# Kernel optimization log

Hardware: AMD Instinct MI355X
Metric: run time of the kernel (lower is better)

The kernel has to match this reference:

```python
import jax, jax.numpy as jnp
import numpy as np

N_NODES = 100000   # ntoken
D = 128            # ninp
N_EDGES = 1600000  # n_nodes * avg_degree(16)


def setup_inputs() -> dict:
    key = jax.random.key(0)
    k0, k1, k2, k3 = jax.random.split(key, 4)
    # nn.Embedding weight, xavier_normal_ init; row 0 is padding_idx -> zeros
    emb = jax.random.normal(k0, (N_NODES, D), jnp.float32) * np.float32(np.sqrt(2.0 / (N_NODES + D)))
    emb = emb.at[0].set(0.0)
    # GCNConv weights (glorot) and biases (zeros), as in torch_geometric defaults
    W1 = jax.random.normal(k1, (D, 2 * D), jnp.float32) * np.float32(np.sqrt(2.0 / (D + 2 * D)))
    b1 = jnp.zeros((2 * D,), jnp.float32)
    W2 = jax.random.normal(k2, (2 * D, D), jnp.float32) * np.float32(np.sqrt(2.0 / (2 * D + D)))
    b2 = jnp.zeros((D,), jnp.float32)
    edge_index = jax.random.randint(k3, (2, N_EDGES), 0, N_NODES, dtype=jnp.int64)
    return {"emb": emb, "W1": W1, "b1": b1, "W2": W2, "b2": b2, "edge_index": edge_index}


def gcn_conv(x, W, b, src, dst, n):
    """torch_geometric GCNConv: add self-loops, sym deg^{-1/2} norm, edge_weight=1."""
    h = x @ W  # [n, out]
    loop = jnp.arange(n, dtype=src.dtype)
    src2 = jnp.concatenate([src, loop])
    dst2 = jnp.concatenate([dst, loop])
    # degree computed at destination (col) including self-loops
    deg = jax.ops.segment_sum(jnp.ones_like(src2, dtype=h.dtype), dst2, num_segments=n)
    dinv = jnp.where(deg > 0, jax.lax.rsqrt(deg), 0.0)
    norm = dinv[src2] * dinv[dst2]  # [E+n]
    msg = h[src2] * norm[:, None]   # gather + scale (memory-bound)
    out = jax.ops.segment_sum(msg, dst2, num_segments=n)  # scatter-add
    return out + b


def reference(emb, W1, b1, W2, b2, edge_index):
    src, dst = edge_index[0], edge_index[1]
    n = emb.shape[0]
    h = gcn_conv(emb, W1, b1, src, dst, n)   # [N, 2D]; dropout = identity (eval)
    out = gcn_conv(h, W2, b2, src, dst, n)   # [N, D]
    return out
```

## Files before the change

### kernel.cpp

```cpp
#include <hip/hip_runtime.h>

static constexpr int D = 128;
static constexpr int CAP = 64;
static constexpr int NSLICE = 8;
static constexpr int CHUNK = 4096;

typedef __attribute__((ext_vector_type(8))) short bf16x8;
typedef __attribute__((ext_vector_type(4))) float f32x4;
typedef __attribute__((ext_vector_type(4))) int iv4;

__device__ inline unsigned bf16rne(float f) {
  unsigned u = __float_as_uint(f);
  return (u + 0x7FFFu + ((u >> 16) & 1u)) >> 16;
}

__global__ __launch_bounds__(256) void k_wprep(const float* __restrict__ W1,
                                               const float* __restrict__ W2,
                                               const float* __restrict__ b1,
                                               uint4* __restrict__ Wp,
                                               float* __restrict__ c2) {
  int cb = blockIdx.x;
  int tid = threadIdx.x;
  if (cb < 8) {
    int t = cb * 256 + tid;
    int l = t & 63, g = t >> 6;
    int ct = g >> 2, ks = g & 3;
    int col = ct * 16 + (l & 15);
    int k0 = ks * 32 + (l >> 4) * 8;
    unsigned r[4];
    #pragma unroll
    for (int jj = 0; jj < 4; ++jj) {
      float lo = 0.f, hi = 0.f;
      for (int m = 0; m < 256; ++m) {
        float w2v = W2[(size_t)m * D + col];
        lo = fmaf(W1[(size_t)(k0 + 2 * jj) * 256 + m], w2v, lo);
        hi = fmaf(W1[(size_t)(k0 + 2 * jj + 1) * 256 + m], w2v, hi);
      }
      r[jj] = bf16rne(lo) | (bf16rne(hi) << 16);
    }
    Wp[t] = make_uint4(r[0], r[1], r[2], r[3]);
  } else if (tid < D) {
    float a2 = 0.f;
    for (int m = 0; m < 256; ++m) a2 = fmaf(b1[m], W2[(size_t)m * D + tid], a2);
    c2[tid] = a2;
  }
}

__global__ __launch_bounds__(256) void k_combo(
    const int* __restrict__ src, const int* __restrict__ dst,
    int* __restrict__ cnt, int* __restrict__ ell,
    const float4* __restrict__ emb4, const uint4* __restrict__ Wp,
    ushort* __restrict__ G16, int e, int n, int fillblocks) {
  const int bid = blockIdx.x;
  const int tid = threadIdx.x;

  if (bid < fillblocks) {
    const int slice = bid % NSLICE;
    const int chunk = bid / NSLICE;
    const int lo = (int)((long long)n * slice / NSLICE);
    const int hi = (int)((long long)n * (slice + 1) / NSLICE);
    const int cbase = chunk * CHUNK;
    #pragma unroll
    for (int i = 0; i < 4; ++i) {
      int idx = cbase + i * 1024 + tid * 4;
      if (idx + 4 <= e) {
        iv4 d4 = __builtin_nontemporal_load((const iv4*)(dst + idx));
        iv4 s4 = __builtin_nontemporal_load((const iv4*)(src + idx));
        if (d4.x >= lo && d4.x < hi) { int p = atomicAdd(&cnt[d4.x], 1); if (p < CAP) ell[(size_t)d4.x * CAP + p] = s4.x; }
        if (d4.y >= lo && d4.y < hi) { int p = atomicAdd(&cnt[d4.y], 1); if (p < CAP) ell[(size_t)d4.y * CAP + p] = s4.y; }
        if (d4.z >= lo && d4.z < hi) { int p = atomicAdd(&cnt[d4.z], 1); if (p < CAP) ell[(size_t)d4.z * CAP + p] = s4.z; }
        if (d4.w >= lo && d4.w < hi) { int p = atomicAdd(&cnt[d4.w], 1); if (p < CAP) ell[(size_t)d4.w * CAP + p] = s4.w; }
      } else {
        for (int k = idx; k < e && k < idx + 4; ++k) {
          int s = src[k], d = dst[k];
          if (d >= lo && d < hi) { int p = atomicAdd(&cnt[d], 1); if (p < CAP) ell[(size_t)d * CAP + p] = s; }
        }
      }
    }
  } else {
    const int gb = bid - fillblocks;
    const int wv = tid >> 6;
    const int l = tid & 63;
    const int row0 = gb * 64 + wv * 16;
    const int rA = row0 + (l & 15);
    const int kb = l >> 4;

    bf16x8 afr[4];
    #pragma unroll
    for (int ks = 0; ks < 4; ++ks) {
      bf16x8 a = 0;
      if (rA < n) {
        float4 v0 = emb4[(size_t)rA * 32 + ks * 8 + kb * 2];
        float4 v1 = emb4[(size_t)rA * 32 + ks * 8 + kb * 2 + 1];
        a[0] = (short)bf16rne(v0.x); a[1] = (short)bf16rne(v0.y);
        a[2] = (short)bf16rne(v0.z); a[3] = (short)bf16rne(v0.w);
        a[4] = (short)bf16rne(v1.x); a[5] = (short)bf16rne(v1.y);
        a[6] = (short)bf16rne(v1.z); a[7] = (short)bf16rne(v1.w);
      }
      afr[ks] = a;
    }

    #pragma unroll
    for (int ct = 0; ct < 8; ++ct) {
      f32x4 acc = {0.f, 0.f, 0.f, 0.f};
      #pragma unroll
      for (int ks = 0; ks < 4; ++ks) {
        bf16x8 bfr = *reinterpret_cast<const bf16x8*>(Wp + (size_t)(ct * 4 + ks) * 64 + l);
        acc = __builtin_amdgcn_mfma_f32_16x16x32_bf16(afr[ks], bfr, acc, 0, 0, 0);
      }
      int col = ct * 16 + (l & 15);
      #pragma unroll
      for (int r = 0; r < 4; ++r) {
        int row = row0 + kb * 4 + r;
        if (row < n) G16[(size_t)row * D + col] = (ushort)bf16rne(acc[r]);
      }
    }
  }
}

template<bool OUT32>
__global__ __launch_bounds__(256) void k_agg16(const uint2* __restrict__ x,
                                               const int* __restrict__ cnt,
                                               const int* __restrict__ ell,
                                               const float* __restrict__ addv,
                                               uint2* __restrict__ y16,
                                               float4* __restrict__ y32, int n) {
  int t = blockIdx.x * blockDim.x + threadIdx.x;
  int node = t >> 5, lane = t & 31;
  if (node >= n) return;
  int deg = cnt[node];
  float dd = rsqrtf(1.0f + (float)deg);
  int m = deg < CAP ? deg : CAP;
  const int* row = ell + (size_t)node * CAP;

  uint2 qv = x[(size_t)node * 32 + lane];
  float4 acc;
  acc.x = __uint_as_float(qv.x << 16) * dd;
  acc.y = __uint_as_float(qv.x & 0xFFFF0000u) * dd;
  acc.z = __uint_as_float(qv.y << 16) * dd;
  acc.w = __uint_as_float(qv.y & 0xFFFF0000u) * dd;

#define ACC4(Q, W)                                                         \
  acc.x = fmaf(__uint_as_float((Q).x << 16), (W), acc.x);                  \
  acc.y = fmaf(__uint_as_float((Q).x & 0xFFFF0000u), (W), acc.y);          \
  acc.z = fmaf(__uint_as_float((Q).y << 16), (W), acc.z);                  \
  acc.w = fmaf(__uint_as_float((Q).y & 0xFFFF0000u), (W), acc.w)

  int j = 0;
  for (; j + 8 <= m; j += 8) {
    int4 i0 = *(const int4*)(row + j);
    int4 i1 = *(const int4*)(row + j + 4);
    uint2 q0 = x[(size_t)i0.x * 32 + lane];
    uint2 q1 = x[(size_t)i0.y * 32 + lane];
    uint2 q2 = x[(size_t)i0.z * 32 + lane];
    uint2 q3 = x[(size_t)i0.w * 32 + lane];
    uint2 q4 = x[(size_t)i1.x * 32 + lane];
    uint2 q5 = x[(size_t)i1.y * 32 + lane];
    uint2 q6 = x[(size_t)i1.z * 32 + lane];
    uint2 q7 = x[(size_t)i1.w * 32 + lane];
    float w0 = rsqrtf(1.0f + (float)cnt[i0.x]);
    float w1 = rsqrtf(1.0f + (float)cnt[i0.y]);
    float w2 = rsqrtf(1.0f + (float)cnt[i0.z]);
    float w3 = rsqrtf(1.0f + (float)cnt[i0.w]);
    float w4 = rsqrtf(1.0f + (float)cnt[i1.x]);
    float w5 = rsqrtf(1.0f + (float)cnt[i1.y]);
    float w6 = rsqrtf(1.0f + (float)cnt[i1.z]);
    float w7 = rsqrtf(1.0f + (float)cnt[i1.w]);
    ACC4(q0, w0); ACC4(q1, w1); ACC4(q2, w2); ACC4(q3, w3);
    ACC4(q4, w4); ACC4(q5, w5); ACC4(q6, w6); ACC4(q7, w7);
  }
  for (; j < m; ++j) {
    int s0 = row[j];
    uint2 q0 = x[(size_t)s0 * 32 + lane];
    float w0 = rsqrtf(1.0f + (float)cnt[s0]);
    ACC4(q0, w0);
  }
#undef ACC4

  float4 b = ((const float4*)addv)[lane];
  float4 o;
  o.x = fmaf(acc.x, dd, b.x); o.y = fmaf(acc.y, dd, b.y);
  o.z = fmaf(acc.z, dd, b.z); o.w = fmaf(acc.w, dd, b.w);
  if (OUT32) {
    y32[(size_t)node * 32 + lane] = o;
  } else {
    uint2 p;
    p.x = bf16rne(o.x) | (bf16rne(o.y) << 16);
    p.y = bf16rne(o.z) | (bf16rne(o.w) << 16);
    y16[(size_t)node * 32 + lane] = p;
  }
}

extern "C" void kernel_launch(void* const* d_in, const int* in_sizes, int n_in,
                              void* d_out, int out_size, void* d_ws, size_t ws_size,
                              hipStream_t stream) {
  const float* emb = (const float*)d_in[0];
  const float* W1  = (const float*)d_in[1];
  const float* b1  = (const float*)d_in[2];
  const float* W2  = (const float*)d_in[3];
  const float* b2  = (const float*)d_in[4];
  const int*   ei  = (const int*)d_in[5];

  const int n = in_sizes[0] / D;
  const int e = in_sizes[5] / 2;
  const int* src = ei;
  const int* dst = ei + e;

  const int B = 256;
  const int nchunk = (e + CHUNK - 1) / CHUNK;
  const int fillblocks = nchunk * NSLICE;
  const int gemmblocks = (n + 63) / 64;

  char* ws = (char*)d_ws;
  size_t off = 0;
  auto alloc = [&](size_t bytes) { void* p = ws + off; off = (off + bytes + 255) & ~(size_t)255; return p; };
  int*    cnt = (int*)   alloc((size_t)n * 4);
  int*    ell = (int*)   alloc((size_t)n * CAP * 4);
  uint4*  Wp  = (uint4*) alloc(2048 * 16);
  float*  c2  = (float*) alloc((size_t)D * 4);
  ushort* G16 = (ushort*)alloc((size_t)n * D * 2);
  ushort* H16 = (ushort*)alloc((size_t)n * D * 2);
  float*  out = (float*)d_out;

  k_wprep<<<9, B, 0, stream>>>(W1, W2, b1, Wp, c2);

  (void)hipMemsetAsync(cnt, 0, (size_t)n * 4, stream);
  k_combo<<<fillblocks + gemmblocks, B, 0, stream>>>(src, dst, cnt, ell,
                                                     (const float4*)emb, Wp, G16,
                                                     e, n, fillblocks);

  {
    long long t = (long long)n * 32;
    k_agg16<false><<<(int)((t + B - 1) / B), B, 0, stream>>>(
        (const uint2*)G16, cnt, ell, c2, (uint2*)H16, nullptr, n);
  }
  {
    long long t = (long long)n * 32;
    k_agg16<true><<<(int)((t + B - 1) / B), B, 0, stream>>>(
        (const uint2*)H16, cnt, ell, b2, nullptr, (float4*)out, n);
  }
}
```

Before: 270.9 us.

## Fuse first aggregation with combined-weight GEMM, aggregate before transform

New measurement: 283.9 us. 4.8% more time.

```diff
diff --git a/kernel.cpp b/kernel.cpp
--- a/kernel.cpp
+++ b/kernel.cpp
@@ -14,43 +14,13 @@
   return (u + 0x7FFFu + ((u >> 16) & 1u)) >> 16;
 }
 
-__global__ __launch_bounds__(256) void k_wprep(const float* __restrict__ W1,
-                                               const float* __restrict__ W2,
-                                               const float* __restrict__ b1,
-                                               uint4* __restrict__ Wp,
-                                               float* __restrict__ c2) {
-  int cb = blockIdx.x;
-  int tid = threadIdx.x;
-  if (cb < 8) {
-    int t = cb * 256 + tid;
-    int l = t & 63, g = t >> 6;
-    int ct = g >> 2, ks = g & 3;
-    int col = ct * 16 + (l & 15);
-    int k0 = ks * 32 + (l >> 4) * 8;
-    unsigned r[4];
-    #pragma unroll
-    for (int jj = 0; jj < 4; ++jj) {
-      float lo = 0.f, hi = 0.f;
-      for (int m = 0; m < 256; ++m) {
-        float w2v = W2[(size_t)m * D + col];
-        lo = fmaf(W1[(size_t)(k0 + 2 * jj) * 256 + m], w2v, lo);
-        hi = fmaf(W1[(size_t)(k0 + 2 * jj + 1) * 256 + m], w2v, hi);
-      }
-      r[jj] = bf16rne(lo) | (bf16rne(hi) << 16);
-    }
-    Wp[t] = make_uint4(r[0], r[1], r[2], r[3]);
-  } else if (tid < D) {
-    float a2 = 0.f;
-    for (int m = 0; m < 256; ++m) a2 = fmaf(b1[m], W2[(size_t)m * D + tid], a2);
-    c2[tid] = a2;
-  }
-}
-
 __global__ __launch_bounds__(256) void k_combo(
     const int* __restrict__ src, const int* __restrict__ dst,
     int* __restrict__ cnt, int* __restrict__ ell,
-    const float4* __restrict__ emb4, const uint4* __restrict__ Wp,
-    ushort* __restrict__ G16, int e, int n, int fillblocks) {
+    const float4* __restrict__ emb4, uint2* __restrict__ E16,
+    const float* __restrict__ W1, const float* __restrict__ W2,
+    const float* __restrict__ b1, uint4* __restrict__ Wp, float* __restrict__ c2,
+    int e, int n, int n4, int fillblocks, int ncvt) {
   const int bid = blockIdx.x;
   const int tid = threadIdx.x;
 
@@ -77,54 +47,160 @@
         }
       }
     }
+  } else if (bid < fillblocks + ncvt) {
+    int i0 = (bid - fillblocks) * 1024 + tid;
+    #pragma unroll
+    for (int k = 0; k < 4; ++k) {
+      int i = i0 + k * 256;
+      if (i < n4) {
+        float4 v = emb4[i];
+        uint2 r;
+        r.x = bf16rne(v.x) | (bf16rne(v.y) << 16);
+        r.y = bf16rne(v.z) | (bf16rne(v.w) << 16);
+        E16[i] = r;
+      }
+    }
   } else {
-    const int gb = bid - fillblocks;
-    const int wv = tid >> 6;
-    const int l = tid & 63;
-    const int row0 = gb * 64 + wv * 16;
-    const int rA = row0 + (l & 15);
-    const int kb = l >> 4;
-
-    bf16x8 afr[4];
+    int cb = bid - fillblocks - ncvt;
+    if (cb < 8) {
+      int t = cb * 256 + tid;
+      int l = t & 63, g = t >> 6;
+      int ct = g >> 2, ks = g & 3;
+      int col = ct * 16 + (l & 15);
+      int k0 = ks * 32 + (l >> 4) * 8;
+      unsigned r[4];
+      #pragma unroll
+      for (int jj = 0; jj < 4; ++jj) {
+        float lo = 0.f, hi = 0.f;
+        for (int m = 0; m < 256; ++m) {
+          float w2v = W2[(size_t)m * D + col];
+          lo = fmaf(W1[(size_t)(k0 + 2 * jj) * 256 + m], w2v, lo);
+          hi = fmaf(W1[(size_t)(k0 + 2 * jj + 1) * 256 + m], w2v, hi);
+        }
+        r[jj] = bf16rne(lo) | (bf16rne(hi) << 16);
+      }
+      Wp[t] = make_uint4(r[0], r[1], r[2], r[3]);
+    } else if (tid < D) {
+      float a2 = 0.f;
+      for (int m = 0; m < 256; ++m) a2 = fmaf(b1[m], W2[(size_t)m * D + tid], a2);
+      c2[tid] = a2;
+    }
+  }
+}
+
+__global__ __launch_bounds__(256) void k_agg1(const uint2* __restrict__ x,
+                                              const int* __restrict__ cnt,
+                                              const int* __restrict__ ell,
+                                              const uint4* __restrict__ Wp,
+                                              const float* __restrict__ c2,
+                                              ushort* __restrict__ H16, int n) {
+  __shared__ uint2 sm[16][33];
+  const int tid = threadIdx.x;
+  sm[8 + (tid >> 5)][tid & 31] = make_uint2(0u, 0u);
+
+  const int node8 = tid >> 5, lane = tid & 31;
+  const int node = blockIdx.x * 8 + node8;
+
+  if (node < n) {
+    int deg = cnt[node];
+    float dd = rsqrtf(1.0f + (float)deg);
+    int m = deg < CAP ? deg : CAP;
+    const int* row = ell + (size_t)node * CAP;
+
+    uint2 qv = x[(size_t)node * 32 + lane];
+    float4 acc;
+    acc.x = __uint_as_float(qv.x << 16) * dd;
+    acc.y = __uint_as_float(qv.x & 0xFFFF0000u) * dd;
+    acc.z = __uint_as_float(qv.y << 16) * dd;
+    acc.w = __uint_as_float(qv.y & 0xFFFF0000u) * dd;
+
+#define ACC4(Q, W)                                                         \
+    acc.x = fmaf(__uint_as_float((Q).x << 16), (W), acc.x);                \
+    acc.y = fmaf(__uint_as_float((Q).x & 0xFFFF0000u), (W), acc.y);        \
+    acc.z = fmaf(__uint_as_float((Q).y << 16), (W), acc.z);                \
+    acc.w = fmaf(__uint_as_float((Q).y & 0xFFFF0000u), (W), acc.w)
+
+    int j = 0;
+    for (; j + 8 <= m; j += 8) {
+      int4 i0 = *(const int4*)(row + j);
+      int4 i1 = *(const int4*)(row + j + 4);
+      uint2 q0 = x[(size_t)i0.x * 32 + lane];
+      uint2 q1 = x[(size_t)i0.y * 32 + lane];
+      uint2 q2 = x[(size_t)i0.z * 32 + lane];
+      uint2 q3 = x[(size_t)i0.w * 32 + lane];
+      uint2 q4 = x[(size_t)i1.x * 32 + lane];
+      uint2 q5 = x[(size_t)i1.y * 32 + lane];
+      uint2 q6 = x[(size_t)i1.z * 32 + lane];
+      uint2 q7 = x[(size_t)i1.w * 32 + lane];
+      float w0 = rsqrtf(1.0f + (float)cnt[i0.x]);
+      float w1 = rsqrtf(1.0f + (float)cnt[i0.y]);
+      float w2 = rsqrtf(1.0f + (float)cnt[i0.z]);
+      float w3 = rsqrtf(1.0f + (float)cnt[i0.w]);
+      float w4 = rsqrtf(1.0f + (float)cnt[i1.x]);
+      float w5 = rsqrtf(1.0f + (float)cnt[i1.y]);
+      float w6 = rsqrtf(1.0f + (float)cnt[i1.z]);
+      float w7 = rsqrtf(1.0f + (float)cnt[i1.w]);
+      ACC4(q0, w0); ACC4(q1, w1); ACC4(q2, w2); ACC4(q3, w3);
+      ACC4(q4, w4); ACC4(q5, w5); ACC4(q6, w6); ACC4(q7, w7);
+    }
+    for (; j < m; ++j) {
+      int s0 = row[j];
+      uint2 q0 = x[(size_t)s0 * 32 + lane];
+      float w0 = rsqrtf(1.0f + (float)cnt[s0]);
+      ACC4(q0, w0);
+    }
+#undef ACC4
+
+    uint2 p;
+    p.x = bf16rne(acc.x * dd) | (bf16rne(acc.y * dd) << 16);
+    p.y = bf16rne(acc.z * dd) | (bf16rne(acc.w * dd) << 16);
+    sm[node8][lane] = p;
+  } else {
+    sm[node8][lane] = make_uint2(0u, 0u);
+  }
+  __syncthreads();
+
+  const int w = tid >> 6;
+  const int l = tid & 63;
+  const int arow = l & 15;
+  const int kb = l >> 4;
+
+  bf16x8 afr[4];
+  #pragma unroll
+  for (int ks = 0; ks < 4; ++ks) {
+    uint2 a0 = sm[arow][ks * 8 + kb * 2];
+    uint2 a1 = sm[arow][ks * 8 + kb * 2 + 1];
+    uint4 av = make_uint4(a0.x, a0.y, a1.x, a1.y);
+    afr[ks] = *reinterpret_cast<bf16x8*>(&av);
+  }
+
+  #pragma unroll
+  for (int cti = 0; cti < 2; ++cti) {
+    int ct = w + cti * 4;
+    f32x4 acc = {0.f, 0.f, 0.f, 0.f};
     #pragma unroll
     for (int ks = 0; ks < 4; ++ks) {
-      bf16x8 a = 0;
-      if (rA < n) {
-        float4 v0 = emb4[(size_t)rA * 32 + ks * 8 + kb * 2];
-        float4 v1 = emb4[(size_t)rA * 32 + ks * 8 + kb * 2 + 1];
-        a[0] = (short)bf16rne(v0.x); a[1] = (short)bf16rne(v0.y);
-        a[2] = (short)bf16rne(v0.z); a[3] = (short)bf16rne(v0.w);
-        a[4] = (short)bf16rne(v1.x); a[5] = (short)bf16rne(v1.y);
-        a[6] = (short)bf16rne(v1.z); a[7] = (short)bf16rne(v1.w);
+      bf16x8 bfr = *reinterpret_cast<const bf16x8*>(Wp + (size_t)(ct * 4 + ks) * 64 + l);
+      acc = __builtin_amdgcn_mfma_f32_16x16x32_bf16(afr[ks], bfr, acc, 0, 0, 0);
+    }
+    int col = ct * 16 + (l & 15);
+    float cb = c2[col];
+    #pragma unroll
+    for (int r = 0; r < 4; ++r) {
+      int row = kb * 4 + r;
+      if (row < 8) {
+        int nd = blockIdx.x * 8 + row;
+        if (nd < n) H16[(size_t)nd * D + col] = (ushort)bf16rne(acc[r] + cb);
       }
-      afr[ks] = a;
-    }
-
-    #pragma unroll
-    for (int ct = 0; ct < 8; ++ct) {
-      f32x4 acc = {0.f, 0.f, 0.f, 0.f};
-      #pragma unroll
-      for (int ks = 0; ks < 4; ++ks) {
-        bf16x8 bfr = *reinterpret_cast<const bf16x8*>(Wp + (size_t)(ct * 4 + ks) * 64 + l);
-        acc = __builtin_amdgcn_mfma_f32_16x16x32_bf16(afr[ks], bfr, acc, 0, 0, 0);
-      }
-      int col = ct * 16 + (l & 15);
-      #pragma unroll
-      for (int r = 0; r < 4; ++r) {
-        int row = row0 + kb * 4 + r;
-        if (row < n) G16[(size_t)row * D + col] = (ushort)bf16rne(acc[r]);
-      }
-    }
-  }
-}
-
-template<bool OUT32>
-__global__ __launch_bounds__(256) void k_agg16(const uint2* __restrict__ x,
-                                               const int* __restrict__ cnt,
-                                               const int* __restrict__ ell,
-                                               const float* __restrict__ addv,
-                                               uint2* __restrict__ y16,
-                                               float4* __restrict__ y32, int n) {
+    }
+  }
+}
+
+__global__ __launch_bounds__(256) void k_agg2(const uint2* __restrict__ x,
+                                              const int* __restrict__ cnt,
+                                              const int* __restrict__ ell,
+                                              const float* __restrict__ b2,
+                                              float4* __restrict__ y, int n) {
   int t = blockIdx.x * blockDim.x + threadIdx.x;
   int node = t >> 5, lane = t & 31;
   if (node >= n) return;
@@ -177,18 +253,11 @@
   }
 #undef ACC4
 
-  float4 b = ((const float4*)addv)[lane];
+  float4 b = ((const float4*)b2)[lane];
   float4 o;
   o.x = fmaf(acc.x, dd, b.x); o.y = fmaf(acc.y, dd, b.y);
   o.z = fmaf(acc.z, dd, b.z); o.w = fmaf(acc.w, dd, b.w);
-  if (OUT32) {
-    y32[(size_t)node * 32 + lane] = o;
-  } else {
-    uint2 p;
-    p.x = bf16rne(o.x) | (bf16rne(o.y) << 16);
-    p.y = bf16rne(o.z) | (bf16rne(o.w) << 16);
-    y16[(size_t)node * 32 + lane] = p;
-  }
+  y[(size_t)node * 32 + lane] = o;
 }
 
 extern "C" void kernel_launch(void* const* d_in, const int* in_sizes, int n_in,
@@ -209,7 +278,8 @@
   const int B = 256;
   const int nchunk = (e + CHUNK - 1) / CHUNK;
   const int fillblocks = nchunk * NSLICE;
-  const int gemmblocks = (n + 63) / 64;
+  const int n4 = n * 32;
+  const int ncvt = (n4 + 1023) / 1024;
 
   char* ws = (char*)d_ws;
   size_t off = 0;
@@ -218,25 +288,21 @@
   int*    ell = (int*)   alloc((size_t)n * CAP * 4);
   uint4*  Wp  = (uint4*) alloc(2048 * 16);
   float*  c2  = (float*) alloc((size_t)D * 4);
-  ushort* G16 = (ushort*)alloc((size_t)n * D * 2);
+  uint2*  E16 = (uint2*) alloc((size_t)n * 32 * 8);
   ushort* H16 = (ushort*)alloc((size_t)n * D * 2);
   float*  out = (float*)d_out;
 
-  k_wprep<<<9, B, 0, stream>>>(W1, W2, b1, Wp, c2);
-
   (void)hipMemsetAsync(cnt, 0, (size_t)n * 4, stream);
-  k_combo<<<fillblocks + gemmblocks, B, 0, stream>>>(src, dst, cnt, ell,
-                                                     (const float4*)emb, Wp, G16,
-                                                     e, n, fillblocks);
+  k_combo<<<fillblocks + ncvt + 9, B, 0, stream>>>(src, dst, cnt, ell,
+                                                   (const float4*)emb, E16,
+                                                   W1, W2, b1, Wp, c2,
+                                                   e, n, n4, fillblocks, ncvt);
+
+  k_agg1<<<(n + 7) / 8, B, 0, stream>>>(E16, cnt, ell, Wp, c2, H16, n);
 
   {
     long long t = (long long)n * 32;
-    k_agg16<false><<<(int)((t + B - 1) / B), B, 0, stream>>>(
-        (const uint2*)G16, cnt, ell, c2, (uint2*)H16, nullptr, n);
-  }
-  {
-    long long t = (long long)n * 32;
-    k_agg16<true><<<(int)((t + B - 1) / B), B, 0, stream>>>(
-        (const uint2*)H16, cnt, ell, b2, nullptr, (float4*)out, n);
-  }
-}
+    k_agg2<<<(int)((t + B - 1) / B), B, 0, stream>>>((const uint2*)H16, cnt, ell, b2,
+                                                     (float4*)out, n);
+  }
+}
```
